# Optimization experiments

Measured on AMD Instinct MI355X. Metric: run time of the kernel, lower is better.

Reference implementation:

```python
import jax, jax.numpy as jnp
import numpy as np

B, DIM, H, W = 32, 384, 32, 32
ORDER = 5
DIMS = [DIM // 2**i for i in range(ORDER)][::-1]  # [24,48,96,192,384]
SUM_DIMS = sum(DIMS)                               # 744 == 2*DIM - DIMS[0]
SCALE = 1.0 / 3.0
EPS = 1e-5


def setup_inputs() -> dict:
    key = jax.random.key(0)
    ks = jax.random.split(key, 32)

    def n(k, shape, s=0.02):
        return jax.random.normal(k, shape, jnp.float32) * s

    inp = {}
    inp['x'] = jax.random.normal(ks[0], (B, DIM, H, W), jnp.float32)
    # norm1: LayerNorm([dim, H, W]) -> per-element affine
    inp['ln1_w'] = jnp.ones((DIM, H, W), jnp.float32) + n(ks[1], (DIM, H, W))
    inp['ln1_b'] = n(ks[2], (DIM, H, W))
    # gnconv params
    inp['proj_in_w'] = n(ks[3], (2 * DIM, DIM))   # 1x1 conv stored as [O,C]
    inp['proj_in_b'] = n(ks[4], (2 * DIM,))
    inp['dw_w'] = n(ks[5], (SUM_DIMS, 1, 7, 7))   # depthwise 7x7
    inp['dw_b'] = n(ks[6], (SUM_DIMS,))
    for i in range(ORDER - 1):
        inp[f'pw{i}_w'] = n(ks[7 + 2 * i], (DIMS[i + 1], DIMS[i]))
        inp[f'pw{i}_b'] = n(ks[8 + 2 * i], (DIMS[i + 1],))
    inp['proj_out_w'] = n(ks[15], (DIM, DIM))
    inp['proj_out_b'] = n(ks[16], (DIM,))
    # norm2 + MLP
    inp['ln2_w'] = jnp.ones((DIM,), jnp.float32) + n(ks[17], (DIM,))
    inp['ln2_b'] = n(ks[18], (DIM,))
    inp['fc1_w'] = n(ks[19], (4 * DIM, DIM))
    inp['fc1_b'] = n(ks[20], (4 * DIM,))
    inp['fc2_w'] = n(ks[21], (DIM, 4 * DIM))
    inp['fc2_b'] = n(ks[22], (DIM,))
    # layer scales
    inp['gamma1'] = 1e-6 * jnp.ones((DIM,), jnp.float32)
    inp['gamma2'] = 1e-6 * jnp.ones((DIM,), jnp.float32)
    return inp


def _conv1x1(x, w, b):
    # x: [B,C,H,W], w: [O,C] -> [B,O,H,W]
    return jnp.einsum('bchw,oc->bohw', x, w) + b[None, :, None, None]


def _dwconv7(x, w, b):
    y = jax.lax.conv_general_dilated(
        x, w, window_strides=(1, 1), padding=[(3, 3), (3, 3)],
        dimension_numbers=('NCHW', 'OIHW', 'NCHW'),
        feature_group_count=x.shape[1])
    return y + b[None, :, None, None]


def reference(x, ln1_w, ln1_b, proj_in_w, proj_in_b, dw_w, dw_b,
              pw0_w, pw0_b, pw1_w, pw1_b, pw2_w, pw2_b, pw3_w, pw3_b,
              proj_out_w, proj_out_b, ln2_w, ln2_b,
              fc1_w, fc1_b, fc2_w, fc2_b, gamma1, gamma2):
    # ---- norm1: LayerNorm over (C,H,W) jointly ----
    mu = x.mean(axis=(1, 2, 3), keepdims=True)
    var = x.var(axis=(1, 2, 3), keepdims=True)
    h = (x - mu) * jax.lax.rsqrt(var + EPS) * ln1_w[None] + ln1_b[None]

    # ---- gnconv (recursive gated conv) ----
    fused = _conv1x1(h, proj_in_w, proj_in_b)          # [B, 2*DIM, H, W]
    pwa = fused[:, :DIMS[0]]
    abc = fused[:, DIMS[0]:]                            # [B, SUM_DIMS, H, W]
    dw = _dwconv7(abc, dw_w, dw_b) * SCALE
    dw_list = jnp.split(dw, np.cumsum(DIMS)[:-1].tolist(), axis=1)
    y = pwa * dw_list[0]
    for i, (wp, bp) in enumerate([(pw0_w, pw0_b), (pw1_w, pw1_b), (pw2_w, pw2_b), (pw3_w, pw3_b)]):
        y = _conv1x1(y, wp, bp) * dw_list[i + 1]
    y = _conv1x1(y, proj_out_w, proj_out_b)             # [B, DIM, H, W]

    x = x + gamma1[None, :, None, None] * y             # residual 1 (drop_path=0 -> identity)

    # ---- ConvNeXt-style MLP, channels-last ----
    h = jnp.transpose(x, (0, 2, 3, 1))                  # [B,H,W,C]
    mu2 = h.mean(axis=-1, keepdims=True)
    var2 = h.var(axis=-1, keepdims=True)
    h = (h - mu2) * jax.lax.rsqrt(var2 + EPS) * ln2_w + ln2_b
    h = jnp.einsum('bhwc,oc->bhwo', h, fc1_w) + fc1_b
    h = jax.nn.gelu(h, approximate=False)               # torch GELU default = erf
    h = jnp.einsum('bhwc,oc->bhwo', h, fc2_w) + fc2_b
    h = gamma2 * h
    h = jnp.transpose(h, (0, 3, 1, 2))                  # back to NCHW
    return x + h
```

## Files before the change

kernel.cpp:

```cpp
#include <hip/hip_runtime.h>
#include <math.h>

#define HW 1024
#define CDIM 384
#define NB 32
#define MTOT (NB * HW)
#define EPS 1e-5f

typedef unsigned short u16;
typedef short s8v __attribute__((ext_vector_type(8)));
typedef short s4v __attribute__((ext_vector_type(4)));
typedef float f4v __attribute__((ext_vector_type(4)));

union U8 { s8v v; u16 u[8]; };

__device__ __forceinline__ float bf2f(u16 u) {
  union { float f; unsigned int i; } x; x.i = ((unsigned int)u) << 16; return x.f;
}
__device__ __forceinline__ u16 f2bf(float f) {
  union { float f; unsigned int i; } x; x.f = f;
  unsigned int r = (x.i + 0x7FFFu + ((x.i >> 16) & 1u)) >> 16;
  return (u16)r;
}
__device__ __forceinline__ float gelu_exact(float v) {
  return 0.5f * v * (1.f + erff(v * 0.70710678118654752f));
}

__device__ __forceinline__ void gload16(const u16* g, u16* l) {
  __builtin_amdgcn_global_load_lds(
      (const __attribute__((address_space(1))) unsigned int*)(unsigned long long)(const void*)g,
      (__attribute__((address_space(3))) unsigned int*)(unsigned int)(unsigned long long)(void*)l,
      16, 0, 0);
}

__global__ __launch_bounds__(256) void k_statsA(const float* __restrict__ x,
                                                float* __restrict__ part) {
  int blk = blockIdx.x;
  const float4* xb = (const float4*)(x + (size_t)blk * 12288);
  float s = 0.f, s2 = 0.f;
  for (int i = threadIdx.x; i < 3072; i += 256) {
    float4 v = xb[i];
    s += v.x + v.y + v.z + v.w;
    s2 += v.x * v.x + v.y * v.y + v.z * v.z + v.w * v.w;
  }
  __shared__ float ls[256], ls2[256];
  ls[threadIdx.x] = s; ls2[threadIdx.x] = s2;
  __syncthreads();
  for (int off = 128; off > 0; off >>= 1) {
    if (threadIdx.x < off) {
      ls[threadIdx.x] += ls[threadIdx.x + off];
      ls2[threadIdx.x] += ls2[threadIdx.x + off];
    }
    __syncthreads();
  }
  if (threadIdx.x == 0) { part[blk * 2] = ls[0]; part[blk * 2 + 1] = ls2[0]; }
}

__global__ void k_statsB(const float* __restrict__ part, float* __restrict__ stats) {
  int b = threadIdx.x;
  if (b >= 32) return;
  float s = 0.f, s2 = 0.f;
  for (int i = 0; i < 32; i++) {
    s += part[(b * 32 + i) * 2];
    s2 += part[(b * 32 + i) * 2 + 1];
  }
  const float inv_n = 1.f / (CDIM * HW);
  float m = s * inv_n;
  stats[b] = m;
  stats[32 + b] = rsqrtf(s2 * inv_n - m * m + EPS);
}

__global__ __launch_bounds__(256) void k_cvtwE(const float* __restrict__ piw,
                                               const float* __restrict__ pow_,
                                               const float* __restrict__ p0w,
                                               const float* __restrict__ p1w,
                                               const float* __restrict__ p2w,
                                               const float* __restrict__ p3w,
                                               u16* __restrict__ dst) {
  int i = blockIdx.x * 256 + threadIdx.x;
  if (i < 294912) dst[i] = f2bf(piw[i]);
  else if (i < 442368) dst[i] = f2bf(pow_[i - 294912]);
  else if (i < 443904) { int j = i - 442368, o = j >> 5, k = j & 31;
    dst[i] = (k < 24) ? f2bf(p0w[o * 24 + k]) : (u16)0; }
  else if (i < 450048) { int j = i - 443904, o = j >> 6, k = j & 63;
    dst[i] = (k < 48) ? f2bf(p1w[o * 48 + k]) : (u16)0; }
  else if (i < 468480) dst[i] = f2bf(p2w[i - 450048]);
  else dst[i] = f2bf(p3w[i - 468480]);
}

__global__ __launch_bounds__(256) void k_cvtwL(const float* __restrict__ fc1,
                                               const float* __restrict__ fc2,
                                               u16* __restrict__ dst) {
  int i = blockIdx.x * 256 + threadIdx.x;
  if (i < 589824) dst[i] = f2bf(fc1[i]);
  else dst[i] = f2bf(fc2[i - 589824]);
}

__global__ __launch_bounds__(256) void k_trln1(const float* __restrict__ x,
                                               const float* __restrict__ lnw,
                                               const float* __restrict__ lnb,
                                               const float* __restrict__ stats,
                                               u16* __restrict__ xn,
                                               u16* __restrict__ hn) {
  int pt = blockIdx.x, ct = blockIdx.y, b = blockIdx.z;
  __shared__ float xs[32][33], hs[32][33];
  float m = stats[b], rs = stats[32 + b];
  int t = threadIdx.x;
  int ci0 = t >> 5, pi = t & 31;
#pragma unroll
  for (int it = 0; it < 4; it++) {
    int ci = ci0 + it * 8;
    int c = ct * 32 + ci;
    size_t src = ((size_t)b * CDIM + c) * HW + pt * 32 + pi;
    size_t wsrc = (size_t)c * HW + pt * 32 + pi;
    float xv = x[src];
    xs[ci][pi] = xv;
    hs[ci][pi] = (xv - m) * rs * lnw[wsrc] + lnb[wsrc];
  }
  __syncthreads();
  int co = t & 31, pr0 = t >> 5;
#pragma unroll
  for (int it = 0; it < 4; it++) {
    int pr = pr0 + it * 8;
    int p = pt * 32 + pr;
    int c = ct * 32 + co;
    size_t dst = ((size_t)b * HW + p) * CDIM + c;
    xn[dst] = f2bf(xs[co][pr]);
    hn[dst] = f2bf(hs[co][pr]);
  }
}

template <int MODE>
__global__ __launch_bounds__(256)
void k_mfma(const u16* __restrict__ A, const u16* __restrict__ Wb,
            const float* __restrict__ bias, void* __restrict__ Out,
            const u16* __restrict__ gate, int gate_off,
            const u16* __restrict__ resbf, const float* __restrict__ gvec,
            int m_base, int K, int O, int OS) {
  __shared__ u16 As[4096];
  __shared__ u16 Bs[4096];
  const int t = threadIdx.x;
  const int m0 = blockIdx.x * 128, o0 = blockIdx.y * 128;
  const int w = t >> 6, l = t & 63;
  const int wm = (w >> 1) * 64, wn = (w & 1) * 64;
  const int lr = l & 15, lk = (l >> 4) * 8;

  const u16* gA = A + (size_t)(m0 + w * 32 + (l >> 2)) * K + (l & 3) * 8;
  const u16* gB = Wb + (size_t)(o0 + w * 32 + (l >> 2)) * K + (l & 3) * 8;
  u16* ldsA0 = As + w * 1024;
  u16* ldsB0 = Bs + w * 1024;

  f4v acc[4][4];
#pragma unroll
  for (int i = 0; i < 4; i++)
#pragma unroll
    for (int j = 0; j < 4; j++) acc[i][j] = {};

  for (int k0 = 0; k0 < K; k0 += 32) {
    gload16(gA + k0, ldsA0);
    gload16(gA + 16 * K + k0, ldsA0 + 512);
    gload16(gB + k0, ldsB0);
    gload16(gB + 16 * K + k0, ldsB0 + 512);
    __syncthreads();
    s8v a[4], b[4];
#pragma unroll
    for (int mi = 0; mi < 4; mi++)
      a[mi] = *(const s8v*)&As[(wm + mi * 16 + lr) * 32 + lk];
#pragma unroll
    for (int fj = 0; fj < 4; fj++)
      b[fj] = *(const s8v*)&Bs[(wn + fj * 16 + lr) * 32 + lk];
#pragma unroll
    for (int mi = 0; mi < 4; mi++)
#pragma unroll
      for (int fj = 0; fj < 4; fj++)
        acc[mi][fj] = __builtin_amdgcn_mfma_f32_16x16x32_bf16(a[mi], b[fj], acc[mi][fj], 0, 0, 0);
    __syncthreads();
  }

  const int orow = (l >> 4) * 4;
#pragma unroll
  for (int mi = 0; mi < 4; mi++) {
    int p = m0 + wm + mi * 16 + orow;
#pragma unroll
    for (int fj = 0; fj < 4; fj++) {
      int o = o0 + wn + fj * 16 + lr;
      if (MODE == 1 && o >= OS) continue;
      float bo = (MODE == 1 && o >= O) ? 0.f : bias[o];
      float gv = (MODE == 2 || MODE == 4) ? gvec[o] : 0.f;
      if (MODE == 4) {
        int gp = m_base + p;
        float4 st;
        float* stp = &st.x;
#pragma unroll
        for (int r = 0; r < 4; r++)
          stp[r] = bf2f(resbf[(size_t)(gp + r) * CDIM + o]) + gv * (acc[mi][fj][r] + bo);
        int bb = gp >> 10, hw = gp & 1023;
        *(float4*)((float*)Out + ((size_t)bb * CDIM + o) * HW + hw) = st;
      } else {
#pragma unroll
        for (int r = 0; r < 4; r++) {
          float val = acc[mi][fj][r] + bo;
          size_t rowi = (size_t)(p + r);
          if (MODE == 0) {
            ((u16*)Out)[rowi * OS + o] = f2bf(val);
          } else if (MODE == 1) {
            float g = (o < O) ? bf2f(gate[rowi * 744 + gate_off + o]) : 0.f;
            ((u16*)Out)[rowi * OS + o] = (o < O) ? f2bf(val * g) : (u16)0;
          } else if (MODE == 2) {
            size_t idx = rowi * CDIM + o;
            ((u16*)Out)[idx] = f2bf(bf2f(resbf[idx]) + gv * val);
          } else if (MODE == 3) {
            ((u16*)Out)[rowi * OS + o] = f2bf(gelu_exact(val));
          }
        }
      }
    }
  }
}

__global__ __launch_bounds__(256) void k_dwconv(const u16* __restrict__ fused,
                                                const float* __restrict__ w,
                                                const float* __restrict__ bias,
                                                u16* __restrict__ dwo,
                                                u16* __restrict__ y0) {
  const int ys = blockIdx.x;
  const int cb = blockIdx.y;
  const int b = blockIdx.z;
  __shared__ u16 tile[14][32][32];
  __shared__ float wk[32][49];
  const int c0 = cb * 32;
  const int t = threadIdx.x;
  for (int i = t; i < 32 * 49; i += 256) {
    int c = i / 49, k = i % 49;
    wk[c][k] = (c0 + c < 744) ? w[(size_t)(c0 + c) * 49 + k] : 0.f;
  }
  const int lx = t >> 3, cq = (t & 7) * 4;
  const int fch = 24 + c0 + cq;
#pragma unroll
  for (int yy = 0; yy < 14; yy++) {
    int y = ys * 8 - 3 + yy;
    s4v v = {0, 0, 0, 0};
    if (y >= 0 && y < 32 && fch < 768)
      v = *(const s4v*)(fused + ((size_t)b * HW + y * 32 + lx) * 768 + fch);
    *(s4v*)&tile[yy][lx][cq] = v;
  }
  __syncthreads();
  const int c = t & 31, dy = t >> 5;
  const bool valid = (c0 + c) < 744;
  const float bv = valid ? bias[c0 + c] : 0.f;
  float acc[32];
#pragma unroll
  for (int x = 0; x < 32; x++) acc[x] = 0.f;
#pragma unroll
  for (int ky = 0; ky < 7; ky++) {
    int yy = dy + ky;
    float r[38];
    r[0] = r[1] = r[2] = 0.f; r[35] = r[36] = r[37] = 0.f;
#pragma unroll
    for (int x = 0; x < 32; x++) r[x + 3] = bf2f(tile[yy][x][c]);
#pragma unroll
    for (int kx = 0; kx < 7; kx++) {
      float wv = wk[c][ky * 7 + kx];
#pragma unroll
      for (int x = 0; x < 32; x++) acc[x] += r[x + kx] * wv;
    }
  }
  const int yout = ys * 8 + dy;
  const size_t prow = (size_t)b * HW + yout * 32;
  if (valid) {
#pragma unroll
    for (int x = 0; x < 32; x++)
      dwo[(prow + x) * 744 + c0 + c] = f2bf((acc[x] + bv) * (1.f / 3.f));
  }
  if (cb == 0) {
#pragma unroll
    for (int x = 0; x < 32; x++) {
      u16 o = 0;
      if (c < 24)
        o = f2bf(bf2f(fused[(prow + x) * 768 + c]) * ((acc[x] + bv) * (1.f / 3.f)));
      y0[(prow + x) * 32 + c] = o;
    }
  }
}

__global__ __launch_bounds__(256) void k_ln2(const u16* __restrict__ xm,
                                             const float* __restrict__ w,
                                             const float* __restrict__ bb,
                                             u16* __restrict__ outp) {
  int row = blockIdx.x * 4 + (threadIdx.x >> 6);
  int l = threadIdx.x & 63;
  float v[8];
  float s = 0.f, s2 = 0.f;
  if (l < 48) {
    U8 u;
    u.v = *(const s8v*)(xm + (size_t)row * CDIM + l * 8);
#pragma unroll
    for (int i = 0; i < 8; i++) {
      v[i] = bf2f(u.u[i]);
      s += v[i]; s2 += v[i] * v[i];
    }
  }
#pragma unroll
  for (int off = 32; off > 0; off >>= 1) {
    s += __shfl_xor(s, off);
    s2 += __shfl_xor(s2, off);
  }
  const float inv_n = 1.f / CDIM;
  float m = s * inv_n;
  float rs = rsqrtf(s2 * inv_n - m * m + EPS);
  if (l < 48) {
    U8 res;
#pragma unroll
    for (int i = 0; i < 8; i++) {
      int c = l * 8 + i;
      res.u[i] = f2bf((v[i] - m) * rs * w[c] + bb[c]);
    }
    *(s8v*)(outp + (size_t)row * CDIM + l * 8) = res.v;
  }
}

extern "C" void kernel_launch(void* const* d_in, const int* in_sizes, int n_in,
                              void* d_out, int out_size, void* d_ws, size_t ws_size,
                              hipStream_t stream) {
  const float* x          = (const float*)d_in[0];
  const float* ln1_w      = (const float*)d_in[1];
  const float* ln1_b      = (const float*)d_in[2];
  const float* proj_in_w  = (const float*)d_in[3];
  const float* proj_in_b  = (const float*)d_in[4];
  const float* dw_w       = (const float*)d_in[5];
  const float* dw_b       = (const float*)d_in[6];
  const float* pw0_w      = (const float*)d_in[7];
  const float* pw0_b      = (const float*)d_in[8];
  const float* pw1_w      = (const float*)d_in[9];
  const float* pw1_b      = (const float*)d_in[10];
  const float* pw2_w      = (const float*)d_in[11];
  const float* pw2_b      = (const float*)d_in[12];
  const float* pw3_w      = (const float*)d_in[13];
  const float* pw3_b      = (const float*)d_in[14];
  const float* proj_out_w = (const float*)d_in[15];
  const float* proj_out_b = (const float*)d_in[16];
  const float* ln2_w      = (const float*)d_in[17];
  const float* ln2_b      = (const float*)d_in[18];
  const float* fc1_w      = (const float*)d_in[19];
  const float* fc1_b      = (const float*)d_in[20];
  const float* fc2_w      = (const float*)d_in[21];
  const float* fc2_b      = (const float*)d_in[22];
  const float* gamma1     = (const float*)d_in[23];
  const float* gamma2     = (const float*)d_in[24];
  float* out = (float*)d_out;

  const size_t MiB = 1ull << 20;
  char* ws = (char*)d_ws;
  u16* xn   = (u16*)(ws + 0);
  u16* hn   = (u16*)(ws + 24 * MiB);
  u16* fus  = (u16*)(ws + 48 * MiB);
  u16* dw   = (u16*)(ws + 96 * MiB);
  u16* wE   = (u16*)(ws + 142 * MiB + 512 * 1024);
  float* stats = (float*)(ws + 143 * MiB + 768 * 1024);
  float* part  = stats + 64;
  u16* y0 = (u16*)(ws + 24 * MiB);
  u16* y1 = (u16*)(ws + 26 * MiB);
  u16* y2 = (u16*)(ws + 30 * MiB);
  u16* y3 = (u16*)(ws + 36 * MiB);
  u16* y4 = (u16*)(ws + 48 * MiB);
  u16* xmid = (u16*)(ws + 72 * MiB);
  u16* ln2h = (u16*)(ws + 0);
  u16* fc1b = (u16*)(ws + 24 * MiB);
  u16* fc2b = fc1b + 589824;
  u16* h1 = (u16*)(ws + 96 * MiB);

  u16* piw_b = wE;
  u16* pow_b = wE + 294912;
  u16* pw0b  = wE + 442368;
  u16* pw1b  = wE + 443904;
  u16* pw2b  = wE + 450048;
  u16* pw3b  = wE + 468480;

  k_statsA<<<1024, 256, 0, stream>>>(x, part);
  k_statsB<<<1, 64, 0, stream>>>(part, stats);
  k_cvtwE<<<2118, 256, 0, stream>>>(proj_in_w, proj_out_w, pw0_w, pw1_w, pw2_w, pw3_w, wE);
  k_trln1<<<dim3(32, 12, NB), 256, 0, stream>>>(x, ln1_w, ln1_b, stats, xn, hn);
  k_mfma<0><<<dim3(256, 6), 256, 0, stream>>>(hn, piw_b, proj_in_b, fus, nullptr, 0,
                                              nullptr, nullptr, 0, 384, 768, 768);
  k_dwconv<<<dim3(4, 24, NB), 256, 0, stream>>>(fus, dw_w, dw_b, dw, y0);
  k_mfma<1><<<dim3(256, 1), 256, 0, stream>>>(y0, pw0b, pw0_b, y1, dw, 24, nullptr,
                                              nullptr, 0, 32, 48, 64);
  k_mfma<1><<<dim3(256, 1), 256, 0, stream>>>(y1, pw1b, pw1_b, y2, dw, 72, nullptr,
                                              nullptr, 0, 64, 96, 96);
  k_mfma<1><<<dim3(256, 2), 256, 0, stream>>>(y2, pw2b, pw2_b, y3, dw, 168, nullptr,
                                              nullptr, 0, 96, 192, 192);
  k_mfma<1><<<dim3(256, 3), 256, 0, stream>>>(y3, pw3b, pw3_b, y4, dw, 360, nullptr,
                                              nullptr, 0, 192, 384, 384);
  k_mfma<2><<<dim3(256, 3), 256, 0, stream>>>(y4, pow_b, proj_out_b, xmid, nullptr, 0,
                                              xn, gamma1, 0, 384, 384, 384);
  k_ln2<<<MTOT / 4, 256, 0, stream>>>(xmid, ln2_w, ln2_b, ln2h);
  k_cvtwL<<<4608, 256, 0, stream>>>(fc1_w, fc2_w, fc1b);
  for (int ch = 0; ch < 2; ch++) {
    int m_base = ch * 16384;
    k_mfma<3><<<dim3(128, 12), 256, 0, stream>>>(ln2h + (size_t)m_base * CDIM, fc1b,
                                                 fc1_b, h1, nullptr, 0, nullptr, nullptr,
                                                 0, 384, 1536, 1536);
    k_mfma<4><<<dim3(128, 3), 256, 0, stream>>>(h1, fc2b, fc2_b, out, nullptr, 0, xmid,
                                                gamma2, m_base, 1536, 384, 384);
  }
}
```

Baseline: 440.4 us.

## Retile depthwise conv: 64 channels, 4 rows, half-row x per thread

The 7x7 depthwise conv now uses 512-thread blocks covering 64 channels and 4 output rows. Each thread computes 16 x positions instead of 32, and the shared tile is loaded with 16-byte vector reads. The smaller per-thread accumulator array is meant to cut register pressure and raise occupancy, and the wider channel slice gives coalesced loads. The cost is a larger halo, since 10 input rows are loaded per 4 output rows instead of 14 per 8, plus bounds checks inside the inner gather.

```diff
diff --git a/kernel.cpp b/kernel.cpp
--- a/kernel.cpp
+++ b/kernel.cpp
@@ -218,7 +218,7 @@
   }
 }
 
-__global__ __launch_bounds__(256) void k_dwconv(const u16* __restrict__ fused,
+__global__ __launch_bounds__(512) void k_dwconv(const u16* __restrict__ fused,
                                                 const float* __restrict__ w,
                                                 const float* __restrict__ bias,
                                                 u16* __restrict__ dwo,
@@ -226,55 +226,61 @@
   const int ys = blockIdx.x;
   const int cb = blockIdx.y;
   const int b = blockIdx.z;
-  __shared__ u16 tile[14][32][32];
-  __shared__ float wk[32][49];
-  const int c0 = cb * 32;
+  __shared__ u16 tile[10][32][64];
+  __shared__ float wk[64][49];
+  const int c0 = cb * 64;
   const int t = threadIdx.x;
-  for (int i = t; i < 32 * 49; i += 256) {
-    int c = i / 49, k = i % 49;
-    wk[c][k] = (c0 + c < 744) ? w[(size_t)(c0 + c) * 49 + k] : 0.f;
-  }
-  const int lx = t >> 3, cq = (t & 7) * 4;
-  const int fch = 24 + c0 + cq;
-#pragma unroll
-  for (int yy = 0; yy < 14; yy++) {
-    int y = ys * 8 - 3 + yy;
-    s4v v = {0, 0, 0, 0};
-    if (y >= 0 && y < 32 && fch < 768)
-      v = *(const s4v*)(fused + ((size_t)b * HW + y * 32 + lx) * 768 + fch);
-    *(s4v*)&tile[yy][lx][cq] = v;
+  for (int i = t; i < 64 * 49; i += 512) {
+    int cc = i / 49, k = i % 49;
+    wk[cc][k] = (c0 + cc < 744) ? w[(size_t)(c0 + cc) * 49 + k] : 0.f;
+  }
+  {
+    const int lx = (t >> 3) & 31, co = (t & 7) * 8;
+    const int fch = 24 + c0 + co;
+    for (int yy = t >> 8; yy < 10; yy += 2) {
+      int y = ys * 4 - 3 + yy;
+      s8v v = {0, 0, 0, 0, 0, 0, 0, 0};
+      if (y >= 0 && y < 32 && fch < 768)
+        v = *(const s8v*)(fused + ((size_t)b * HW + y * 32 + lx) * 768 + fch);
+      *(s8v*)&tile[yy][lx][co] = v;
+    }
   }
   __syncthreads();
-  const int c = t & 31, dy = t >> 5;
+  const int c = t & 63;
+  const int dy = (t >> 6) & 3;
+  const int xh = t >> 8;
+  const int xb0 = xh * 16;
   const bool valid = (c0 + c) < 744;
   const float bv = valid ? bias[c0 + c] : 0.f;
-  float acc[32];
-#pragma unroll
-  for (int x = 0; x < 32; x++) acc[x] = 0.f;
+  float acc[16];
+#pragma unroll
+  for (int x = 0; x < 16; x++) acc[x] = 0.f;
 #pragma unroll
   for (int ky = 0; ky < 7; ky++) {
     int yy = dy + ky;
-    float r[38];
-    r[0] = r[1] = r[2] = 0.f; r[35] = r[36] = r[37] = 0.f;
-#pragma unroll
-    for (int x = 0; x < 32; x++) r[x + 3] = bf2f(tile[yy][x][c]);
+    float r[22];
+#pragma unroll
+    for (int i = 0; i < 22; i++) {
+      int xg = xb0 + i - 3;
+      r[i] = (xg >= 0 && xg < 32) ? bf2f(tile[yy][xg][c]) : 0.f;
+    }
 #pragma unroll
     for (int kx = 0; kx < 7; kx++) {
       float wv = wk[c][ky * 7 + kx];
 #pragma unroll
-      for (int x = 0; x < 32; x++) acc[x] += r[x + kx] * wv;
-    }
-  }
-  const int yout = ys * 8 + dy;
-  const size_t prow = (size_t)b * HW + yout * 32;
+      for (int x = 0; x < 16; x++) acc[x] += r[x + kx] * wv;
+    }
+  }
+  const int yout = ys * 4 + dy;
+  const size_t prow = (size_t)b * HW + yout * 32 + xb0;
   if (valid) {
 #pragma unroll
-    for (int x = 0; x < 32; x++)
+    for (int x = 0; x < 16; x++)
       dwo[(prow + x) * 744 + c0 + c] = f2bf((acc[x] + bv) * (1.f / 3.f));
   }
-  if (cb == 0) {
-#pragma unroll
-    for (int x = 0; x < 32; x++) {
+  if (cb == 0 && c < 32) {
+#pragma unroll
+    for (int x = 0; x < 16; x++) {
       u16 o = 0;
       if (c < 24)
         o = f2bf(bf2f(fused[(prow + x) * 768 + c]) * ((acc[x] + bv) * (1.f / 3.f)));
@@ -382,7 +388,7 @@
   k_trln1<<<dim3(32, 12, NB), 256, 0, stream>>>(x, ln1_w, ln1_b, stats, xn, hn);
   k_mfma<0><<<dim3(256, 6), 256, 0, stream>>>(hn, piw_b, proj_in_b, fus, nullptr, 0,
                                               nullptr, nullptr, 0, 384, 768, 768);
-  k_dwconv<<<dim3(4, 24, NB), 256, 0, stream>>>(fus, dw_w, dw_b, dw, y0);
+  k_dwconv<<<dim3(8, 12, NB), 512, 0, stream>>>(fus, dw_w, dw_b, dw, y0);
   k_mfma<1><<<dim3(256, 1), 256, 0, stream>>>(y0, pw0b, pw0_b, y1, dw, 24, nullptr,
                                               nullptr, 0, 32, 48, 64);
   k_mfma<1><<<dim3(256, 1), 256, 0, stream>>>(y1, pw1b, pw1_b, y2, dw, 72, nullptr,
```

Result: slower. 518.3 us (+17.7%).
